# Kernel optimization log

Measured on AMD Instinct MI355X. Metric: run time of the kernel, lower is better.

Reference implementation:

```python
import jax, jax.numpy as jnp
import numpy as np

N_NODES = 50000
N_EDGES = 800000
IN_DIM = 128
HIDDEN = 64
HEADS = 4
EPS = 1e-5
NEG_SLOPE = 0.2  # PyG GATConv default


def setup_inputs() -> dict:
    key = jax.random.key(0)
    ks = jax.random.split(key, 12)
    s = 0.1
    x = jax.random.normal(ks[0], (N_NODES, IN_DIM), jnp.float32)
    edge_index = jax.random.randint(ks[1], (2, N_EDGES), 0, N_NODES, dtype=jnp.int64)
    return {
        "x": x,
        "edge_index": edge_index,
        # BatchNorm1d(input_dim)
        "gamma1": jnp.ones((IN_DIM,), jnp.float32),
        "beta1": jnp.zeros((IN_DIM,), jnp.float32),
        # GATConv(IN_DIM, HIDDEN, heads=HEADS, concat=True)
        "W1": jax.random.normal(ks[2], (IN_DIM, HEADS * HIDDEN), jnp.float32) * s,
        "att_src1": jax.random.normal(ks[3], (HEADS, HIDDEN), jnp.float32) * s,
        "att_dst1": jax.random.normal(ks[4], (HEADS, HIDDEN), jnp.float32) * s,
        "bias1": jnp.zeros((HEADS * HIDDEN,), jnp.float32),
        # BatchNorm1d(hidden*heads)
        "gamma2": jnp.ones((HEADS * HIDDEN,), jnp.float32),
        "beta2": jnp.zeros((HEADS * HIDDEN,), jnp.float32),
        # GATConv(hidden*heads, HIDDEN, heads=HEADS, concat=False)
        "W2": jax.random.normal(ks[5], (HEADS * HIDDEN, HEADS * HIDDEN), jnp.float32) * s,
        "att_src2": jax.random.normal(ks[6], (HEADS, HIDDEN), jnp.float32) * s,
        "att_dst2": jax.random.normal(ks[7], (HEADS, HIDDEN), jnp.float32) * s,
        "bias2": jnp.zeros((HIDDEN,), jnp.float32),
    }


def batchnorm(x, gamma, beta):
    # training-mode BatchNorm1d: biased variance over the batch dim
    m = x.mean(axis=0)
    v = x.var(axis=0)
    return (x - m) * jax.lax.rsqrt(v + EPS) * gamma + beta


def gat_conv(h, src, dst, W, att_src, att_dst, bias, concat):
    n = h.shape[0]
    hl = (h @ W).reshape(n, HEADS, -1)                 # [N, H, C]
    a_src = (hl * att_src).sum(-1)                     # [N, H]
    a_dst = (hl * att_dst).sum(-1)                     # [N, H]
    e = jax.nn.leaky_relu(a_src[src] + a_dst[dst], NEG_SLOPE)  # [E, H]
    # segment softmax over destination neighborhoods
    e_max = jax.ops.segment_max(e, dst, num_segments=n)
    e = jnp.exp(e - e_max[dst])
    denom = jax.ops.segment_sum(e, dst, num_segments=n)
    alpha = e / denom[dst]                             # [E, H]
    msg = alpha[:, :, None] * hl[src]                  # [E, H, C]
    out = jax.ops.segment_sum(msg, dst, num_segments=n)  # [N, H, C]
    out = out.reshape(n, -1) if concat else out.mean(axis=1)
    return out + bias


def reference(x, edge_index, gamma1, beta1, W1, att_src1, att_dst1, bias1,
              gamma2, beta2, W2, att_src2, att_dst2, bias2):
    n = x.shape[0]
    loop = jnp.arange(n, dtype=edge_index.dtype)
    src = jnp.concatenate([edge_index[0], loop])  # add_self_loops=True
    dst = jnp.concatenate([edge_index[1], loop])
    h = batchnorm(x, gamma1, beta1)
    h = gat_conv(h, src, dst, W1, att_src1, att_dst1, bias1, concat=True)
    h = batchnorm(h, gamma2, beta2)
    h = jax.nn.relu(h)
    h = gat_conv(h, src, dst, W2, att_src2, att_dst2, bias2, concat=False)
    return h
```

## Files before the change

### kernel.cpp

```cpp
#include <hip/hip_runtime.h>

#define N_NODES 50000
#define N_EDGES 800000
#define E_TOT   (N_EDGES + N_NODES)
#define F1      128
#define F2      256
#define EPS     1e-5f
#define SLOPE   0.2f
#define CAP     448
#define SCAN_B  256
#define N_BLKS  ((N_NODES + SCAN_B - 1) / SCAN_B)

typedef __bf16 bf16x8 __attribute__((ext_vector_type(8)));
typedef float  f32x4  __attribute__((ext_vector_type(4)));

__device__ __forceinline__ float bf2f(unsigned short b) {
    return __uint_as_float((unsigned)b << 16);
}

template<int C>
__global__ void bn_stats(const float* __restrict__ X,
                         float* __restrict__ sums, float* __restrict__ sumsq) {
    int t = threadIdx.x;
    float s = 0.f, q = 0.f;
    for (int r = blockIdx.x; r < N_NODES; r += gridDim.x) {
        float v = X[(size_t)r * C + t];
        s += v; q += v * v;
    }
    atomicAdd(&sums[t], s);
    atomicAdd(&sumsq[t], q);
}

__global__ void bn_coef(const float* __restrict__ sums, const float* __restrict__ sumsq,
                        const float* __restrict__ gamma, const float* __restrict__ beta,
                        float* __restrict__ scale, float* __restrict__ shift, int K) {
    int t = blockIdx.x * 64 + threadIdx.x;
    if (t < K) {
        const float invN = 1.f / (float)N_NODES;
        float m  = sums[t] * invN;
        float vv = sumsq[t] * invN - m * m;
        float sc = rsqrtf(vv + EPS) * gamma[t];
        scale[t] = sc;
        shift[t] = fmaf(-m, sc, beta[t]);
    }
}

__global__ void deg_init(int* __restrict__ deg) {
    int i = blockIdx.x * 256 + threadIdx.x;
    if (i < N_NODES) deg[i] = 1;
}
__global__ void deg_count(const int* __restrict__ edst, int* __restrict__ deg) {
    int i = blockIdx.x * 256 + threadIdx.x;
    if (i < N_EDGES) atomicAdd(&deg[edst[i]], 1);
}
__global__ void scan_blocks(const int* __restrict__ deg, int* __restrict__ rowptr,
                            int* __restrict__ bsum) {
    __shared__ int sd[SCAN_B];
    int b = blockIdx.x, t = threadIdx.x;
    int i = b * SCAN_B + t;
    int v = (i < N_NODES) ? deg[i] : 0;
    sd[t] = v;
    __syncthreads();
    for (int off = 1; off < SCAN_B; off <<= 1) {
        int x = (t >= off) ? sd[t - off] : 0;
        __syncthreads();
        sd[t] += x;
        __syncthreads();
    }
    if (i < N_NODES) rowptr[i + 1] = sd[t];
    if (t == SCAN_B - 1) bsum[b] = sd[t];
}
__global__ void scan_totals(int* __restrict__ bsum) {
    __shared__ int sd[SCAN_B];
    int t = threadIdx.x;
    int v = (t < N_BLKS) ? bsum[t] : 0;
    sd[t] = v;
    __syncthreads();
    for (int off = 1; off < SCAN_B; off <<= 1) {
        int x = (t >= off) ? sd[t - off] : 0;
        __syncthreads();
        sd[t] += x;
        __syncthreads();
    }
    if (t < N_BLKS) bsum[t] = sd[t] - v;
}
__global__ void scan_apply(const int* __restrict__ deg, const int* __restrict__ bsum,
                           int* __restrict__ rowptr, int* __restrict__ cursor) {
    int i = blockIdx.x * SCAN_B + threadIdx.x;
    if (i < N_NODES) {
        int r = rowptr[i + 1] + bsum[blockIdx.x];
        rowptr[i + 1] = r;
        cursor[i] = r - deg[i];
        if (i == 0) rowptr[0] = 0;
    }
}
__global__ void fill_csr(const int* __restrict__ esrc, const int* __restrict__ edst,
                         int* __restrict__ cursor, int* __restrict__ col) {
    int i = blockIdx.x * 256 + threadIdx.x;
    if (i < N_EDGES) {
        int p = atomicAdd(&cursor[edst[i]], 1);
        col[p] = esrc[i];
    } else if (i < E_TOT) {
        int n = i - N_EDGES;
        int p = atomicAdd(&cursor[n], 1);
        col[p] = n;
    }
}

template<int K>
__global__ void prep_w(const float* __restrict__ W, __bf16* __restrict__ Wf) {
    int tid = blockIdx.x * 256 + threadIdx.x;
    if (tid >= (K / 32) * 16 * 64) return;
    int lane = tid & 63;
    int nt = (tid >> 6) & 15;
    int ks = tid >> 10;
    int q = lane >> 4, c = lane & 15;
#pragma unroll
    for (int j = 0; j < 8; j++)
        Wf[(size_t)tid * 8 + j] = (__bf16)W[(size_t)(ks * 32 + q * 8 + j) * F2 + nt * 16 + c];
}

template<int K, bool RELU>
__global__ __launch_bounds__(256)
void gemm_mfma(const float* __restrict__ X,
               const float* __restrict__ scale, const float* __restrict__ shift,
               const __bf16* __restrict__ Wf, __bf16* __restrict__ hlb) {
    int t = threadIdx.x;
    int wave = t >> 6, lane = t & 63;
    int q = lane >> 4, c = lane & 15;
    int mrow = (blockIdx.x * 4 + wave) * 32;
    int row0 = mrow + c, row1 = mrow + 16 + c;
    int r0 = row0 < N_NODES ? row0 : N_NODES - 1;
    int r1 = row1 < N_NODES ? row1 : N_NODES - 1;

    f32x4 acc[2][16];
#pragma unroll
    for (int m = 0; m < 2; m++)
#pragma unroll
        for (int nt = 0; nt < 16; nt++) acc[m][nt] = (f32x4){0.f, 0.f, 0.f, 0.f};

    for (int ks = 0; ks < K / 32; ks++) {
        int kb = ks * 32 + q * 8;
        float4 sc0 = *(const float4*)(scale + kb);
        float4 sc1 = *(const float4*)(scale + kb + 4);
        float4 sf0 = *(const float4*)(shift + kb);
        float4 sf1 = *(const float4*)(shift + kb + 4);
        bf16x8 afr[2];
#pragma unroll
        for (int m = 0; m < 2; m++) {
            const float* xp = X + (size_t)(m ? r1 : r0) * K + kb;
            float4 x0 = *(const float4*)xp;
            float4 x1 = *(const float4*)(xp + 4);
            float y0 = fmaf(x0.x, sc0.x, sf0.x);
            float y1 = fmaf(x0.y, sc0.y, sf0.y);
            float y2 = fmaf(x0.z, sc0.z, sf0.z);
            float y3 = fmaf(x0.w, sc0.w, sf0.w);
            float y4 = fmaf(x1.x, sc1.x, sf1.x);
            float y5 = fmaf(x1.y, sc1.y, sf1.y);
            float y6 = fmaf(x1.z, sc1.z, sf1.z);
            float y7 = fmaf(x1.w, sc1.w, sf1.w);
            if (RELU) {
                y0 = fmaxf(y0, 0.f); y1 = fmaxf(y1, 0.f);
                y2 = fmaxf(y2, 0.f); y3 = fmaxf(y3, 0.f);
                y4 = fmaxf(y4, 0.f); y5 = fmaxf(y5, 0.f);
                y6 = fmaxf(y6, 0.f); y7 = fmaxf(y7, 0.f);
            }
            bf16x8 a;
            a[0] = (__bf16)y0; a[1] = (__bf16)y1; a[2] = (__bf16)y2; a[3] = (__bf16)y3;
            a[4] = (__bf16)y4; a[5] = (__bf16)y5; a[6] = (__bf16)y6; a[7] = (__bf16)y7;
            afr[m] = a;
        }
#pragma unroll
        for (int nt = 0; nt < 16; nt++) {
            bf16x8 b = *(const bf16x8*)(Wf + ((size_t)(ks * 16 + nt) * 64 + lane) * 8);
            acc[0][nt] = __builtin_amdgcn_mfma_f32_16x16x32_bf16(afr[0], b, acc[0][nt], 0, 0, 0);
            acc[1][nt] = __builtin_amdgcn_mfma_f32_16x16x32_bf16(afr[1], b, acc[1][nt], 0, 0, 0);
        }
    }
#pragma unroll
    for (int m = 0; m < 2; m++) {
        int rowb = mrow + m * 16 + q * 4;
#pragma unroll
        for (int r = 0; r < 4; r++) {
            int row = rowb + r;
            if (row < N_NODES) {
#pragma unroll
                for (int nt = 0; nt < 16; nt++)
                    hlb[(size_t)row * F2 + nt * 16 + c] = (__bf16)acc[m][nt][r];
            }
        }
    }
}

__global__ __launch_bounds__(256)
void att_dots(const __bf16* __restrict__ hlb,
              const float* __restrict__ att_s, const float* __restrict__ att_d,
              float* __restrict__ a_src, float* __restrict__ a_dst) {
    int t = threadIdx.x;
    int wave = t >> 6, lane = t & 63;
    int n = blockIdx.x * 4 + wave;
    ushort4 hv = ((const ushort4*)(hlb + (size_t)n * F2))[lane];
    float4 as = ((const float4*)att_s)[lane];
    float4 ad = ((const float4*)att_d)[lane];
    float v0 = bf2f(hv.x), v1 = bf2f(hv.y), v2 = bf2f(hv.z), v3 = bf2f(hv.w);
    float vs = v0 * as.x + v1 * as.y + v2 * as.z + v3 * as.w;
    float vd = v0 * ad.x + v1 * ad.y + v2 * ad.z + v3 * ad.w;
#pragma unroll
    for (int off = 1; off < 16; off <<= 1) { vs += __shfl_xor(vs, off); vd += __shfl_xor(vd, off); }
    if ((lane & 15) == 0) {
        int h = lane >> 4;
        a_src[n * 4 + h] = vs;
        a_dst[n * 4 + h] = vd;
    }
}

template<bool MEAN>
__global__ __launch_bounds__(128)
void node_aggr(const int* __restrict__ rowptr, const int* __restrict__ col,
               const float* __restrict__ a_src, const float* __restrict__ a_dst,
               const ushort2* __restrict__ hlb, const float* __restrict__ bias,
               float* __restrict__ out) {
    int n = blockIdx.x, t = threadIdx.x;
    int start = rowptr[n];
    int deg = rowptr[n + 1] - start;
    __shared__ float se[CAP * 4];
    __shared__ int   scol[CAP];
    __shared__ float wred[8];
    __shared__ float sdenom[4];
    int h4 = t & 3;
    float adn = a_dst[n * 4 + h4];
    float local = 0.f;
    bool fits = (deg <= CAP);
    if (fits) {
        for (int i = t; i < deg; i += 128) scol[i] = col[start + i];
        __syncthreads();
        for (int p = t; p < deg * 4; p += 128) {
            int i = p >> 2;
            float v = a_src[scol[i] * 4 + h4] + adn;
            v = v > 0.f ? v : SLOPE * v;
            float e = __expf(v);
            se[p] = e;
            local += e;
        }
    } else {
        for (int p = t; p < deg * 4; p += 128) {
            float v = a_src[col[start + (p >> 2)] * 4 + h4] + adn;
            v = v > 0.f ? v : SLOPE * v;
            local += __expf(v);
        }
    }
#pragma unroll
    for (int off = 4; off < 64; off <<= 1) local += __shfl_xor(local, off);
    if ((t & 63) < 4) wred[(t >> 6) * 4 + h4] = local;
    __syncthreads();
    if (t < 4) sdenom[t] = wred[t] + wred[t + 4];
    __syncthreads();

    int h = t >> 5;
    float rden = 1.f / sdenom[h];
    float acc0 = 0.f, acc1 = 0.f;
    if (fits) {
#pragma unroll 4
        for (int i = 0; i < deg; i++) {
            float alpha = se[i * 4 + h] * rden;
            ushort2 hv = hlb[(size_t)scol[i] * (F2 / 2) + t];
            acc0 = fmaf(alpha, bf2f(hv.x), acc0);
            acc1 = fmaf(alpha, bf2f(hv.y), acc1);
        }
    } else {
        float adh = a_dst[n * 4 + h];
        for (int i = 0; i < deg; i++) {
            int s = col[start + i];
            float v = a_src[s * 4 + h] + adh;
            v = v > 0.f ? v : SLOPE * v;
            float alpha = __expf(v) * rden;
            ushort2 hv = hlb[(size_t)s * (F2 / 2) + t];
            acc0 = fmaf(alpha, bf2f(hv.x), acc0);
            acc1 = fmaf(alpha, bf2f(hv.y), acc1);
        }
    }
    if (MEAN) {
        __shared__ float sred[256];
        sred[2 * t] = acc0; sred[2 * t + 1] = acc1;
        __syncthreads();
        if (t < 64)
            out[(size_t)n * 64 + t] =
                0.25f * (sred[t] + sred[t + 64] + sred[t + 128] + sred[t + 192]) + bias[t];
    } else {
        float2 o; o.x = acc0; o.y = acc1;
        ((float2*)out)[(size_t)n * (F2 / 2) + t] = o;
    }
}

extern "C" void kernel_launch(void* const* d_in, const int* in_sizes, int n_in,
                              void* d_out, int out_size, void* d_ws, size_t ws_size,
                              hipStream_t stream) {
    const float* x        = (const float*)d_in[0];
    const int*   edge     = (const int*)  d_in[1];
    const float* gamma1   = (const float*)d_in[2];
    const float* beta1    = (const float*)d_in[3];
    const float* W1       = (const float*)d_in[4];
    const float* att_src1 = (const float*)d_in[5];
    const float* att_dst1 = (const float*)d_in[6];
    const float* gamma2   = (const float*)d_in[8];
    const float* beta2    = (const float*)d_in[9];
    const float* W2       = (const float*)d_in[10];
    const float* att_src2 = (const float*)d_in[11];
    const float* att_dst2 = (const float*)d_in[12];
    const float* bias2    = (const float*)d_in[13];
    float* out = (float*)d_out;

    const int* esrc = edge;
    const int* edst = edge + N_EDGES;

    float* wsf = (float*)d_ws;
    size_t o = 0;
    __bf16* hlb = (__bf16*)(wsf + o); o += (size_t)N_NODES * F2 / 2;
    float* acc1   = wsf + o; o += (size_t)N_NODES * F2;
    __bf16* Wf1 = (__bf16*)(wsf + o); o += (size_t)F1 * F2 / 2;
    __bf16* Wf2 = (__bf16*)(wsf + o); o += (size_t)F2 * F2 / 2;
    float* a_src1 = wsf + o; o += N_NODES * 4;
    float* a_dst1 = wsf + o; o += N_NODES * 4;
    float* a_src2 = wsf + o; o += N_NODES * 4;
    float* a_dst2 = wsf + o; o += N_NODES * 4;
    float* scale1 = wsf + o; o += F1;
    float* shift1 = wsf + o; o += F1;
    float* scale2 = wsf + o; o += F2;
    float* shift2 = wsf + o; o += F2;
    size_t zstart = o;
    float* sums1  = wsf + o; o += F1;
    float* sumsq1 = wsf + o; o += F1;
    float* sums2  = wsf + o; o += F2;
    float* sumsq2 = wsf + o; o += F2;
    size_t zbytes = (o - zstart) * sizeof(float);
    int* deg    = (int*)(wsf + o); o += N_NODES;
    int* rowptr = (int*)(wsf + o); o += N_NODES + 1;
    int* cursor = (int*)(wsf + o); o += N_NODES;
    int* bsum   = (int*)(wsf + o); o += SCAN_B;
    int* col    = (int*)(wsf + o); o += E_TOT;

    hipMemsetAsync(wsf + zstart, 0, zbytes, stream);

    deg_init   <<<(N_NODES + 255) / 256, 256, 0, stream>>>(deg);
    deg_count  <<<(N_EDGES + 255) / 256, 256, 0, stream>>>(edst, deg);
    scan_blocks<<<N_BLKS, SCAN_B, 0, stream>>>(deg, rowptr, bsum);
    scan_totals<<<1, SCAN_B, 0, stream>>>(bsum);
    scan_apply <<<N_BLKS, SCAN_B, 0, stream>>>(deg, bsum, rowptr, cursor);
    fill_csr   <<<(E_TOT + 255) / 256, 256, 0, stream>>>(esrc, edst, cursor, col);

    prep_w<F1><<<(F1 / 32) * 16 * 64 / 256, 256, 0, stream>>>(W1, Wf1);
    prep_w<F2><<<(F2 / 32) * 16 * 64 / 256, 256, 0, stream>>>(W2, Wf2);

    const int gemm_grid = (N_NODES + 127) / 128;

    bn_stats<F1><<<512, F1, 0, stream>>>(x, sums1, sumsq1);
    bn_coef<<<(F1 + 63) / 64, 64, 0, stream>>>(sums1, sumsq1, gamma1, beta1, scale1, shift1, F1);
    gemm_mfma<F1, false><<<gemm_grid, 256, 0, stream>>>(x, scale1, shift1, Wf1, hlb);
    att_dots<<<N_NODES / 4, 256, 0, stream>>>(hlb, att_src1, att_dst1, a_src1, a_dst1);
    node_aggr<false><<<N_NODES, 128, 0, stream>>>(rowptr, col, a_src1, a_dst1,
                                                  (const ushort2*)hlb, nullptr, acc1);

    bn_stats<F2><<<512, F2, 0, stream>>>(acc1, sums2, sumsq2);
    bn_coef<<<(F2 + 63) / 64, 64, 0, stream>>>(sums2, sumsq2, gamma2, beta2, scale2, shift2, F2);
    gemm_mfma<F2, true><<<gemm_grid, 256, 0, stream>>>(acc1, scale2, shift2, Wf2, hlb);
    att_dots<<<N_NODES / 4, 256, 0, stream>>>(hlb, att_src2, att_dst2, a_src2, a_dst2);
    node_aggr<true><<<N_NODES, 128, 0, stream>>>(rowptr, col, a_src2, a_dst2,
                                                 (const ushort2*)hlb, bias2, out);
}
```

Measured before the change: 499.9 us.

## Fuse attention dots into GEMM, store layer-1 output as bf16, trim CAP

Computes the per-node attention source/destination dot products inside the MFMA GEMM epilogue from the accumulators, which removes the separate att_dots kernels and their re-read of the hidden features. The layer-1 aggregation output is stored as bf16 instead of fp32, halving traffic for the BN-stats and second GEMM reads. Softmax normalization moves out of the edge loop, deg_init is folded into deg_count plus the memset, and CAP drops to 96 to cut shared memory and raise occupancy. In exchange the intermediate loses precision, and high-degree nodes fall to the slower non-cached path. The single-pass column load (scol[t] for t<deg) is still safe because CAP is below the block size.

```diff
diff --git a/kernel.cpp b/kernel.cpp
--- a/kernel.cpp
+++ b/kernel.cpp
@@ -7,7 +7,7 @@
 #define F2      256
 #define EPS     1e-5f
 #define SLOPE   0.2f
-#define CAP     448
+#define CAP     96
 #define SCAN_B  256
 #define N_BLKS  ((N_NODES + SCAN_B - 1) / SCAN_B)
 
@@ -17,14 +17,29 @@
 __device__ __forceinline__ float bf2f(unsigned short b) {
     return __uint_as_float((unsigned)b << 16);
 }
-
-template<int C>
-__global__ void bn_stats(const float* __restrict__ X,
-                         float* __restrict__ sums, float* __restrict__ sumsq) {
+__device__ __forceinline__ unsigned short f2bf(float f) {
+    unsigned u = __float_as_uint(f);
+    u += 0x7fffu + ((u >> 16) & 1u);
+    return (unsigned short)(u >> 16);
+}
+
+__global__ void bn_stats_f32(const float* __restrict__ X,
+                             float* __restrict__ sums, float* __restrict__ sumsq) {
     int t = threadIdx.x;
     float s = 0.f, q = 0.f;
     for (int r = blockIdx.x; r < N_NODES; r += gridDim.x) {
-        float v = X[(size_t)r * C + t];
+        float v = X[(size_t)r * F1 + t];
+        s += v; q += v * v;
+    }
+    atomicAdd(&sums[t], s);
+    atomicAdd(&sumsq[t], q);
+}
+__global__ void bn_stats_bf16(const unsigned short* __restrict__ X,
+                              float* __restrict__ sums, float* __restrict__ sumsq) {
+    int t = threadIdx.x;
+    float s = 0.f, q = 0.f;
+    for (int r = blockIdx.x; r < N_NODES; r += gridDim.x) {
+        float v = bf2f(X[(size_t)r * F2 + t]);
         s += v; q += v * v;
     }
     atomicAdd(&sums[t], s);
@@ -45,13 +60,10 @@
     }
 }
 
-__global__ void deg_init(int* __restrict__ deg) {
-    int i = blockIdx.x * 256 + threadIdx.x;
-    if (i < N_NODES) deg[i] = 1;
-}
 __global__ void deg_count(const int* __restrict__ edst, int* __restrict__ deg) {
     int i = blockIdx.x * 256 + threadIdx.x;
     if (i < N_EDGES) atomicAdd(&deg[edst[i]], 1);
+    else if (i < E_TOT) atomicAdd(&deg[i - N_EDGES], 1);
 }
 __global__ void scan_blocks(const int* __restrict__ deg, int* __restrict__ rowptr,
                             int* __restrict__ bsum) {
@@ -120,11 +132,13 @@
         Wf[(size_t)tid * 8 + j] = (__bf16)W[(size_t)(ks * 32 + q * 8 + j) * F2 + nt * 16 + c];
 }
 
-template<int K, bool RELU>
+template<int K, bool RELU, bool ABF16>
 __global__ __launch_bounds__(256)
-void gemm_mfma(const float* __restrict__ X,
+void gemm_mfma(const void* __restrict__ Xv,
                const float* __restrict__ scale, const float* __restrict__ shift,
-               const __bf16* __restrict__ Wf, __bf16* __restrict__ hlb) {
+               const __bf16* __restrict__ Wf,
+               const float* __restrict__ att_s, const float* __restrict__ att_d,
+               __bf16* __restrict__ hlb, float* __restrict__ a_src, float* __restrict__ a_dst) {
     int t = threadIdx.x;
     int wave = t >> 6, lane = t & 63;
     int q = lane >> 4, c = lane & 15;
@@ -141,33 +155,35 @@
 
     for (int ks = 0; ks < K / 32; ks++) {
         int kb = ks * 32 + q * 8;
-        float4 sc0 = *(const float4*)(scale + kb);
-        float4 sc1 = *(const float4*)(scale + kb + 4);
-        float4 sf0 = *(const float4*)(shift + kb);
-        float4 sf1 = *(const float4*)(shift + kb + 4);
+        float scv[8], sfv[8];
+        *(float4*)scv       = *(const float4*)(scale + kb);
+        *(float4*)(scv + 4) = *(const float4*)(scale + kb + 4);
+        *(float4*)sfv       = *(const float4*)(shift + kb);
+        *(float4*)(sfv + 4) = *(const float4*)(shift + kb + 4);
         bf16x8 afr[2];
 #pragma unroll
         for (int m = 0; m < 2; m++) {
-            const float* xp = X + (size_t)(m ? r1 : r0) * K + kb;
-            float4 x0 = *(const float4*)xp;
-            float4 x1 = *(const float4*)(xp + 4);
-            float y0 = fmaf(x0.x, sc0.x, sf0.x);
-            float y1 = fmaf(x0.y, sc0.y, sf0.y);
-            float y2 = fmaf(x0.z, sc0.z, sf0.z);
-            float y3 = fmaf(x0.w, sc0.w, sf0.w);
-            float y4 = fmaf(x1.x, sc1.x, sf1.x);
-            float y5 = fmaf(x1.y, sc1.y, sf1.y);
-            float y6 = fmaf(x1.z, sc1.z, sf1.z);
-            float y7 = fmaf(x1.w, sc1.w, sf1.w);
-            if (RELU) {
-                y0 = fmaxf(y0, 0.f); y1 = fmaxf(y1, 0.f);
-                y2 = fmaxf(y2, 0.f); y3 = fmaxf(y3, 0.f);
-                y4 = fmaxf(y4, 0.f); y5 = fmaxf(y5, 0.f);
-                y6 = fmaxf(y6, 0.f); y7 = fmaxf(y7, 0.f);
+            int rr = m ? r1 : r0;
+            float y[8];
+            if (ABF16) {
+                const unsigned short* xp = (const unsigned short*)Xv + (size_t)rr * K + kb;
+                uint4 raw = *(const uint4*)xp;
+                y[0] = bf2f(raw.x & 0xffff); y[1] = bf2f(raw.x >> 16);
+                y[2] = bf2f(raw.y & 0xffff); y[3] = bf2f(raw.y >> 16);
+                y[4] = bf2f(raw.z & 0xffff); y[5] = bf2f(raw.z >> 16);
+                y[6] = bf2f(raw.w & 0xffff); y[7] = bf2f(raw.w >> 16);
+            } else {
+                const float* xp = (const float*)Xv + (size_t)rr * K + kb;
+                *(float4*)y       = *(const float4*)xp;
+                *(float4*)(y + 4) = *(const float4*)(xp + 4);
             }
             bf16x8 a;
-            a[0] = (__bf16)y0; a[1] = (__bf16)y1; a[2] = (__bf16)y2; a[3] = (__bf16)y3;
-            a[4] = (__bf16)y4; a[5] = (__bf16)y5; a[6] = (__bf16)y6; a[7] = (__bf16)y7;
+#pragma unroll
+            for (int j = 0; j < 8; j++) {
+                float yy = fmaf(y[j], scv[j], sfv[j]);
+                if (RELU) yy = fmaxf(yy, 0.f);
+                a[j] = (__bf16)yy;
+            }
             afr[m] = a;
         }
 #pragma unroll
@@ -177,6 +193,7 @@
             acc[1][nt] = __builtin_amdgcn_mfma_f32_16x16x32_bf16(afr[1], b, acc[1][nt], 0, 0, 0);
         }
     }
+
 #pragma unroll
     for (int m = 0; m < 2; m++) {
         int rowb = mrow + m * 16 + q * 4;
@@ -190,27 +207,41 @@
             }
         }
     }
-}
-
-__global__ __launch_bounds__(256)
-void att_dots(const __bf16* __restrict__ hlb,
-              const float* __restrict__ att_s, const float* __restrict__ att_d,
-              float* __restrict__ a_src, float* __restrict__ a_dst) {
-    int t = threadIdx.x;
-    int wave = t >> 6, lane = t & 63;
-    int n = blockIdx.x * 4 + wave;
-    ushort4 hv = ((const ushort4*)(hlb + (size_t)n * F2))[lane];
-    float4 as = ((const float4*)att_s)[lane];
-    float4 ad = ((const float4*)att_d)[lane];
-    float v0 = bf2f(hv.x), v1 = bf2f(hv.y), v2 = bf2f(hv.z), v3 = bf2f(hv.w);
-    float vs = v0 * as.x + v1 * as.y + v2 * as.z + v3 * as.w;
-    float vd = v0 * ad.x + v1 * ad.y + v2 * ad.z + v3 * ad.w;
-#pragma unroll
-    for (int off = 1; off < 16; off <<= 1) { vs += __shfl_xor(vs, off); vd += __shfl_xor(vd, off); }
-    if ((lane & 15) == 0) {
-        int h = lane >> 4;
-        a_src[n * 4 + h] = vs;
-        a_dst[n * 4 + h] = vd;
+    float asv[16], adv[16];
+#pragma unroll
+    for (int nt = 0; nt < 16; nt++) { asv[nt] = att_s[nt * 16 + c]; adv[nt] = att_d[nt * 16 + c]; }
+#pragma unroll
+    for (int m = 0; m < 2; m++) {
+#pragma unroll
+        for (int r = 0; r < 4; r++) {
+            int row = mrow + m * 16 + q * 4 + r;
+            float ps0 = 0.f, ps1 = 0.f, ps2 = 0.f, ps3 = 0.f;
+            float pd0 = 0.f, pd1 = 0.f, pd2 = 0.f, pd3 = 0.f;
+#pragma unroll
+            for (int j = 0; j < 4; j++) {
+                ps0 = fmaf(acc[m][j][r],      asv[j],      ps0);
+                ps1 = fmaf(acc[m][4 + j][r],  asv[4 + j],  ps1);
+                ps2 = fmaf(acc[m][8 + j][r],  asv[8 + j],  ps2);
+                ps3 = fmaf(acc[m][12 + j][r], asv[12 + j], ps3);
+                pd0 = fmaf(acc[m][j][r],      adv[j],      pd0);
+                pd1 = fmaf(acc[m][4 + j][r],  adv[4 + j],  pd1);
+                pd2 = fmaf(acc[m][8 + j][r],  adv[8 + j],  pd2);
+                pd3 = fmaf(acc[m][12 + j][r], adv[12 + j], pd3);
+            }
+#pragma unroll
+            for (int off = 1; off < 16; off <<= 1) {
+                ps0 += __shfl_xor(ps0, off); ps1 += __shfl_xor(ps1, off);
+                ps2 += __shfl_xor(ps2, off); ps3 += __shfl_xor(ps3, off);
+                pd0 += __shfl_xor(pd0, off); pd1 += __shfl_xor(pd1, off);
+                pd2 += __shfl_xor(pd2, off); pd3 += __shfl_xor(pd3, off);
+            }
+            if (c == 0 && row < N_NODES) {
+                float4 vs; vs.x = ps0; vs.y = ps1; vs.z = ps2; vs.w = ps3;
+                float4 vd; vd.x = pd0; vd.y = pd1; vd.z = pd2; vd.w = pd3;
+                *(float4*)(a_src + row * 4) = vs;
+                *(float4*)(a_dst + row * 4) = vd;
+            }
+        }
     }
 }
 
@@ -219,7 +250,7 @@
 void node_aggr(const int* __restrict__ rowptr, const int* __restrict__ col,
                const float* __restrict__ a_src, const float* __restrict__ a_dst,
                const ushort2* __restrict__ hlb, const float* __restrict__ bias,
-               float* __restrict__ out) {
+               void* __restrict__ outv) {
     int n = blockIdx.x, t = threadIdx.x;
     int start = rowptr[n];
     int deg = rowptr[n + 1] - start;
@@ -232,7 +263,7 @@
     float local = 0.f;
     bool fits = (deg <= CAP);
     if (fits) {
-        for (int i = t; i < deg; i += 128) scol[i] = col[start + i];
+        if (t < deg) scol[t] = col[start + t];
         __syncthreads();
         for (int p = t; p < deg * 4; p += 128) {
             int i = p >> 2;
@@ -257,15 +288,15 @@
     __syncthreads();
 
     int h = t >> 5;
-    float rden = 1.f / sdenom[h];
+    float rd = 1.f / sdenom[h];
     float acc0 = 0.f, acc1 = 0.f;
     if (fits) {
-#pragma unroll 4
+#pragma unroll 8
         for (int i = 0; i < deg; i++) {
-            float alpha = se[i * 4 + h] * rden;
+            float e = se[i * 4 + h];
             ushort2 hv = hlb[(size_t)scol[i] * (F2 / 2) + t];
-            acc0 = fmaf(alpha, bf2f(hv.x), acc0);
-            acc1 = fmaf(alpha, bf2f(hv.y), acc1);
+            acc0 = fmaf(e, bf2f(hv.x), acc0);
+            acc1 = fmaf(e, bf2f(hv.y), acc1);
         }
     } else {
         float adh = a_dst[n * 4 + h];
@@ -273,22 +304,23 @@
             int s = col[start + i];
             float v = a_src[s * 4 + h] + adh;
             v = v > 0.f ? v : SLOPE * v;
-            float alpha = __expf(v) * rden;
+            float e = __expf(v);
             ushort2 hv = hlb[(size_t)s * (F2 / 2) + t];
-            acc0 = fmaf(alpha, bf2f(hv.x), acc0);
-            acc1 = fmaf(alpha, bf2f(hv.y), acc1);
-        }
-    }
+            acc0 = fmaf(e, bf2f(hv.x), acc0);
+            acc1 = fmaf(e, bf2f(hv.y), acc1);
+        }
+    }
+    acc0 *= rd; acc1 *= rd;
     if (MEAN) {
         __shared__ float sred[256];
         sred[2 * t] = acc0; sred[2 * t + 1] = acc1;
         __syncthreads();
         if (t < 64)
-            out[(size_t)n * 64 + t] =
+            ((float*)outv)[(size_t)n * 64 + t] =
                 0.25f * (sred[t] + sred[t + 64] + sred[t + 128] + sred[t + 192]) + bias[t];
     } else {
-        float2 o; o.x = acc0; o.y = acc1;
-        ((float2*)out)[(size_t)n * (F2 / 2) + t] = o;
+        ushort2 ov; ov.x = f2bf(acc0); ov.y = f2bf(acc1);
+        ((ushort2*)outv)[(size_t)n * (F2 / 2) + t] = ov;
     }
 }
 
@@ -315,8 +347,8 @@
 
     float* wsf = (float*)d_ws;
     size_t o = 0;
-    __bf16* hlb = (__bf16*)(wsf + o); o += (size_t)N_NODES * F2 / 2;
-    float* acc1   = wsf + o; o += (size_t)N_NODES * F2;
+    __bf16* hlb   = (__bf16*)(wsf + o); o += (size_t)N_NODES * F2 / 2;
+    __bf16* acc1b = (__bf16*)(wsf + o); o += (size_t)N_NODES * F2 / 2;
     __bf16* Wf1 = (__bf16*)(wsf + o); o += (size_t)F1 * F2 / 2;
     __bf16* Wf2 = (__bf16*)(wsf + o); o += (size_t)F2 * F2 / 2;
     float* a_src1 = wsf + o; o += N_NODES * 4;
@@ -332,8 +364,8 @@
     float* sumsq1 = wsf + o; o += F1;
     float* sums2  = wsf + o; o += F2;
     float* sumsq2 = wsf + o; o += F2;
+    int* deg    = (int*)(wsf + o); o += N_NODES;
     size_t zbytes = (o - zstart) * sizeof(float);
-    int* deg    = (int*)(wsf + o); o += N_NODES;
     int* rowptr = (int*)(wsf + o); o += N_NODES + 1;
     int* cursor = (int*)(wsf + o); o += N_NODES;
     int* bsum   = (int*)(wsf + o); o += SCAN_B;
@@ -341,8 +373,7 @@
 
     hipMemsetAsync(wsf + zstart, 0, zbytes, stream);
 
-    deg_init   <<<(N_NODES + 255) / 256, 256, 0, stream>>>(deg);
-    deg_count  <<<(N_EDGES + 255) / 256, 256, 0, stream>>>(edst, deg);
+    deg_count  <<<(E_TOT + 255) / 256, 256, 0, stream>>>(edst, deg);
     scan_blocks<<<N_BLKS, SCAN_B, 0, stream>>>(deg, rowptr, bsum);
     scan_totals<<<1, SCAN_B, 0, stream>>>(bsum);
     scan_apply <<<N_BLKS, SCAN_B, 0, stream>>>(deg, bsum, rowptr, cursor);
@@ -353,17 +384,19 @@
 
     const int gemm_grid = (N_NODES + 127) / 128;
 
-    bn_stats<F1><<<512, F1, 0, stream>>>(x, sums1, sumsq1);
+    bn_stats_f32<<<512, F1, 0, stream>>>(x, sums1, sumsq1);
     bn_coef<<<(F1 + 63) / 64, 64, 0, stream>>>(sums1, sumsq1, gamma1, beta1, scale1, shift1, F1);
-    gemm_mfma<F1, false><<<gemm_grid, 256, 0, stream>>>(x, scale1, shift1, Wf1, hlb);
-    att_dots<<<N_NODES / 4, 256, 0, stream>>>(hlb, att_src1, att_dst1, a_src1, a_dst1);
+    gemm_mfma<F1, false, false><<<gemm_grid, 256, 0, stream>>>(x, scale1, shift1, Wf1,
+                                                               att_src1, att_dst1,
+                                                               hlb, a_src1, a_dst1);
     node_aggr<false><<<N_NODES, 128, 0, stream>>>(rowptr, col, a_src1, a_dst1,
-                                                  (const ushort2*)hlb, nullptr, acc1);
-
-    bn_stats<F2><<<512, F2, 0, stream>>>(acc1, sums2, sumsq2);
+                                                  (const ushort2*)hlb, nullptr, acc1b);
+
+    bn_stats_bf16<<<512, F2, 0, stream>>>((const unsigned short*)acc1b, sums2, sumsq2);
     bn_coef<<<(F2 + 63) / 64, 64, 0, stream>>>(sums2, sumsq2, gamma2, beta2, scale2, shift2, F2);
-    gemm_mfma<F2, true><<<gemm_grid, 256, 0, stream>>>(acc1, scale2, shift2, Wf2, hlb);
-    att_dots<<<N_NODES / 4, 256, 0, stream>>>(hlb, att_src2, att_dst2, a_src2, a_dst2);
+    gemm_mfma<F2, true, true><<<gemm_grid, 256, 0, stream>>>(acc1b, scale2, shift2, Wf2,
+                                                             att_src2, att_dst2,
+                                                             hlb, a_src2, a_dst2);
     node_aggr<true><<<N_NODES, 128, 0, stream>>>(rowptr, col, a_src2, a_dst2,
                                                  (const ushort2*)hlb, bias2, out);
 }
```

Result: faster. 488.4 us (-2.3%).
